# Kernel optimization log

Measured on AMD Instinct MI355X. Metric: run time of the kernel, lower is better.

## Reference

```python
import jax, jax.numpy as jnp
import numpy as np

N = 50000          # nodes
E = 800000         # edges per meta-path (avg degree 16)
M = 2              # meta-paths
IN = 256           # in_size
H, D = 4, 64       # heads, out_size per head
HD = H * D
SEM_HID = 128      # SemanticAttention hidden_size
NEG_SLOPE = 0.2    # DGL GATConv default LeakyReLU slope


def setup_inputs() -> dict:
    key = jax.random.key(0)
    ks = jax.random.split(key, 10)
    h = jax.random.normal(ks[0], (N, IN), dtype=jnp.float32)
    src = jax.random.randint(ks[1], (M, E), 0, N, dtype=jnp.int32)
    dst = jax.random.randint(ks[2], (M, E), 0, N, dtype=jnp.int32)
    # per-meta-path GATConv params
    W = jax.random.normal(ks[3], (M, IN, HD), dtype=jnp.float32) * (1.0 / np.sqrt(IN))
    attn_l = jax.random.normal(ks[4], (M, H, D), dtype=jnp.float32) * 0.1
    attn_r = jax.random.normal(ks[5], (M, H, D), dtype=jnp.float32) * 0.1
    # semantic attention params
    sem_w1 = jax.random.normal(ks[6], (HD, SEM_HID), dtype=jnp.float32) * (1.0 / np.sqrt(HD))
    sem_b1 = jnp.zeros((SEM_HID,), dtype=jnp.float32)
    sem_w2 = jax.random.normal(ks[7], (SEM_HID, 1), dtype=jnp.float32) * (1.0 / np.sqrt(SEM_HID))
    return {"h": h, "src": src, "dst": dst, "W": W, "attn_l": attn_l,
            "attn_r": attn_r, "sem_w1": sem_w1, "sem_b1": sem_b1, "sem_w2": sem_w2}


def _gat_conv(h, s, d, W_i, al, ar):
    # h: [N, IN]; s, d: [E] int edge endpoints; returns [N, H*D]
    feat = (h @ W_i).reshape(N, H, D)                       # [N,H,D]
    el = jnp.einsum('nhd,hd->nh', feat, al)                 # [N,H]
    er = jnp.einsum('nhd,hd->nh', feat, ar)                 # [N,H]
    e = jax.nn.leaky_relu(el[s] + er[d], NEG_SLOPE)         # [E,H]
    # edge softmax over incoming edges of each dst node
    m = jax.ops.segment_max(e, d, num_segments=N)           # [N,H]
    m = jax.lax.stop_gradient(jnp.where(jnp.isfinite(m), m, 0.0))
    ex = jnp.exp(e - m[d])                                  # [E,H]
    den = jax.ops.segment_sum(ex, d, num_segments=N)        # [N,H]
    alpha = ex / jnp.maximum(den[d], 1e-9)                  # [E,H]
    msg = alpha[:, :, None] * feat[s]                       # [E,H,D]
    rst = jax.ops.segment_sum(msg, d, num_segments=N)       # [N,H,D] (zero for 0-in-degree)
    return jax.nn.elu(rst).reshape(N, HD)


def reference(h, src, dst, W, attn_l, attn_r, sem_w1, sem_b1, sem_w2):
    embs = [_gat_conv(h, src[i], dst[i], W[i], attn_l[i], attn_r[i]) for i in range(M)]
    z = jnp.stack(embs, axis=1)                             # [N,M,HD]
    # semantic attention: w = mean over nodes of MLP score per meta-path
    w = jnp.einsum('nms,so->mo', jnp.tanh(jnp.einsum('nmd,ds->nms', z, sem_w1) + sem_b1), sem_w2) / N  # [M,1]
    beta = jax.nn.softmax(w, axis=0)                        # [M,1]
    return jnp.einsum('nmd,mo->nd', z, beta)                # [N,HD]
```

## Files before the change

### kernel.cpp

```cpp
#include <hip/hip_runtime.h>
#include <hip/hip_bf16.h>

#define NND 50000
#define NE 800000
#define NM 2
#define INF 256
#define NH 4
#define HDIM 256
#define SHID 128
#define SLOPE 0.2f
#define NB 196

typedef unsigned short u16;
typedef __attribute__((ext_vector_type(8))) short bf16x8;
typedef __attribute__((ext_vector_type(4))) float f32x4;

__device__ __forceinline__ float us2f(u16 u) {
  union { unsigned int i; float f; } v; v.i = ((unsigned int)u) << 16; return v.f;
}
__device__ __forceinline__ u16 f2us(float f) {
  union { float f; unsigned int i; } v; v.f = f;
  unsigned int r = v.i + 0x7FFFu + ((v.i >> 16) & 1u);
  return (u16)(r >> 16);
}

#define GLDS(g, l) __builtin_amdgcn_global_load_lds( \
    (const __attribute__((address_space(1))) unsigned int*)(g), \
    (__attribute__((address_space(3))) unsigned int*)(l), 16, 0, 0)

__global__ __launch_bounds__(256) void kh_cvt(const float* __restrict__ h,
                                              u16* __restrict__ hb) {
  const size_t i = ((size_t)blockIdx.x * 256 + threadIdx.x) * 8;
  float4 a = *(const float4*)(h + i);
  float4 b = *(const float4*)(h + i + 4);
  bf16x8 r;
  r[0] = f2us(a.x); r[1] = f2us(a.y); r[2] = f2us(a.z); r[3] = f2us(a.w);
  r[4] = f2us(b.x); r[5] = f2us(b.y); r[6] = f2us(b.z); r[7] = f2us(b.w);
  *(bf16x8*)(hb + i) = r;
}

__global__ __launch_bounds__(256) void kt_w(const float* __restrict__ W,
                                            u16* __restrict__ Wt) {
  __shared__ u16 tile[64][65];
  const int t = threadIdx.x;
  const int k0 = blockIdx.x * 64, n0 = blockIdx.y * 64;
  const float* Wm = W + (size_t)blockIdx.z * 65536;
  u16* Wtm = Wt + (size_t)blockIdx.z * 65536;
  const int lr = t >> 2, c0 = (t & 3) * 16;
#pragma unroll
  for (int i = 0; i < 16; ++i)
    tile[lr][c0 + i] = f2us(Wm[(size_t)(k0 + lr) * 256 + n0 + c0 + i]);
  __syncthreads();
#pragma unroll
  for (int i = 0; i < 16; ++i)
    Wtm[(size_t)(n0 + lr) * 256 + k0 + c0 + i] = tile[c0 + i][lr];
}

__global__ __launch_bounds__(256) void kt_w1(const float* __restrict__ w1,
                                             u16* __restrict__ w1t) {
  __shared__ u16 tile[64][65];
  const int t = threadIdx.x;
  const int k0 = blockIdx.x * 64, j0 = blockIdx.y * 64;
  const int lr = t >> 2, c0 = (t & 3) * 16;
#pragma unroll
  for (int i = 0; i < 16; ++i)
    tile[lr][c0 + i] = f2us(w1[(size_t)(k0 + lr) * SHID + j0 + c0 + i]);
  __syncthreads();
#pragma unroll
  for (int i = 0; i < 16; ++i)
    w1t[(size_t)(j0 + lr) * 256 + k0 + c0 + i] = tile[c0 + i][lr];
}

__global__ __launch_bounds__(256) void kc_hist(const int* __restrict__ dst,
                                               int* __restrict__ rowptr) {
  int e = blockIdx.x * 256 + threadIdx.x;
  if (e < NE) atomicAdd(rowptr + dst[e] + 1, 1);
}

__global__ __launch_bounds__(256) void ks1(int* __restrict__ rowptr,
                                           int* __restrict__ bsum) {
  __shared__ int wsums[4];
  const int t = threadIdx.x;
  const int i = blockIdx.x * 256 + t + 1;
  int v = (i <= NND) ? rowptr[i] : 0;
  const int lane = t & 63, wid = t >> 6;
#pragma unroll
  for (int o = 1; o < 64; o <<= 1) {
    int u = __shfl_up(v, o, 64);
    if (lane >= o) v += u;
  }
  if (lane == 63) wsums[wid] = v;
  __syncthreads();
  if (t == 0) {
    int s = 0;
#pragma unroll
    for (int w = 0; w < 4; ++w) { int x = wsums[w]; wsums[w] = s; s += x; }
    bsum[blockIdx.x] = s;
  }
  __syncthreads();
  v += wsums[wid];
  if (i <= NND) rowptr[i] = v;
}

__global__ __launch_bounds__(256) void ks2(int* __restrict__ bsum) {
  __shared__ int wsums[4];
  const int t = threadIdx.x;
  const int v0 = (t < NB) ? bsum[t] : 0;
  int v = v0;
  const int lane = t & 63, wid = t >> 6;
#pragma unroll
  for (int o = 1; o < 64; o <<= 1) {
    int u = __shfl_up(v, o, 64);
    if (lane >= o) v += u;
  }
  if (lane == 63) wsums[wid] = v;
  __syncthreads();
  if (t == 0) {
    int s = 0;
#pragma unroll
    for (int w = 0; w < 4; ++w) { int x = wsums[w]; wsums[w] = s; s += x; }
  }
  __syncthreads();
  v += wsums[wid];
  if (t < NB) bsum[t] = v - v0;
}

__global__ __launch_bounds__(256) void ks3(int* __restrict__ rowptr,
                                           const int* __restrict__ bsum) {
  const int i = blockIdx.x * 256 + threadIdx.x + 1;
  if (blockIdx.x > 0 && i <= NND) rowptr[i] += bsum[blockIdx.x];
}

__global__ __launch_bounds__(256) void kc_scatter(
    const int* __restrict__ src, const int* __restrict__ dst,
    int* __restrict__ cursor, int* __restrict__ col,
    const float* __restrict__ el, const float* __restrict__ er,
    float* __restrict__ exps)
{
  int e = blockIdx.x * 256 + threadIdx.x;
  if (e >= NE) return;
  int s = src[e], d = dst[e];
  int pos = atomicAdd(cursor + d, 1);
  col[pos] = s;
  float4 a = *(const float4*)(el + s * 4);
  float4 b = *(const float4*)(er + d * 4);
  float4 r;
  float x;
  x = a.x + b.x; x = x > 0.f ? x : SLOPE * x; r.x = __expf(x);
  x = a.y + b.y; x = x > 0.f ? x : SLOPE * x; r.y = __expf(x);
  x = a.z + b.z; x = x > 0.f ? x : SLOPE * x; r.z = __expf(x);
  x = a.w + b.w; x = x > 0.f ? x : SLOPE * x; r.w = __expf(x);
  *(float4*)(exps + (size_t)pos * 4) = r;
}

__global__ __launch_bounds__(256) void k1_mfma(
    const u16* __restrict__ hb, const u16* __restrict__ Wt,
    u16* __restrict__ feat)
{
  __shared__ u16 As[128 * 32];
  __shared__ u16 Bs[128 * 32];
  const int t = threadIdx.x;
  const int lane = t & 63;
  const int w = t >> 6;
  const int wr = w >> 1, wc = w & 1;
  const int row0 = blockIdx.x * 128;
  const int col0 = blockIdx.y * 128;

  const int sr = t >> 2;
  const int skb = (t & 3) * 8;

  int ra0 = row0 + sr;       if (ra0 >= NND) ra0 = NND - 1;
  int ra1 = row0 + 64 + sr;  if (ra1 >= NND) ra1 = NND - 1;
  const int cb0 = col0 + sr, cb1 = col0 + 64 + sr;

  f32x4 acc[4][4];
#pragma unroll
  for (int i = 0; i < 4; ++i)
#pragma unroll
    for (int j = 0; j < 4; ++j) acc[i][j] = (f32x4){0.f, 0.f, 0.f, 0.f};

  for (int ks = 0; ks < 8; ++ks) {
    const int kb = ks * 32 + skb;
    __syncthreads();
    GLDS(hb + (size_t)ra0 * INF + kb, As + w * 512);
    GLDS(hb + (size_t)ra1 * INF + kb, As + 2048 + w * 512);
    GLDS(Wt + (size_t)cb0 * 256 + kb, Bs + w * 512);
    GLDS(Wt + (size_t)cb1 * 256 + kb, Bs + 2048 + w * 512);
    __syncthreads();
    bf16x8 af[4], bfr[4];
#pragma unroll
    for (int mi = 0; mi < 4; ++mi)
      af[mi] = *(const bf16x8*)(As + (wr * 64 + mi * 16 + (lane & 15)) * 32 + (lane >> 4) * 8);
#pragma unroll
    for (int ni = 0; ni < 4; ++ni)
      bfr[ni] = *(const bf16x8*)(Bs + (wc * 64 + ni * 16 + (lane & 15)) * 32 + (lane >> 4) * 8);
#pragma unroll
    for (int mi = 0; mi < 4; ++mi)
#pragma unroll
      for (int ni = 0; ni < 4; ++ni)
        acc[mi][ni] = __builtin_amdgcn_mfma_f32_16x16x32_bf16(af[mi], bfr[ni], acc[mi][ni], 0, 0, 0);
  }
#pragma unroll
  for (int mi = 0; mi < 4; ++mi) {
    const int r_base = row0 + wr * 64 + mi * 16 + (lane >> 4) * 4;
#pragma unroll
    for (int i = 0; i < 4; ++i) {
      const int r = r_base + i;
      if (r < NND) {
#pragma unroll
        for (int ni = 0; ni < 4; ++ni) {
          const int c = col0 + wc * 64 + ni * 16 + (lane & 15);
          feat[(size_t)r * HDIM + c] = f2us(acc[mi][ni][i]);
        }
      }
    }
  }
}

__global__ __launch_bounds__(256) void k1b_elr(
    const u16* __restrict__ feat,
    const float* __restrict__ al, const float* __restrict__ ar,
    float* __restrict__ el, float* __restrict__ er)
{
  const int n = blockIdx.x * 4 + (threadIdx.x >> 6);
  const int lane = threadIdx.x & 63;
  ushort4 f4 = *(const ushort4*)(feat + (size_t)n * HDIM + lane * 4);
  float4 a4 = *(const float4*)(al + lane * 4);
  float4 r4 = *(const float4*)(ar + lane * 4);
  float fl = us2f(f4.x) * a4.x + us2f(f4.y) * a4.y
           + us2f(f4.z) * a4.z + us2f(f4.w) * a4.w;
  float fr = us2f(f4.x) * r4.x + us2f(f4.y) * r4.y
           + us2f(f4.z) * r4.z + us2f(f4.w) * r4.w;
#pragma unroll
  for (int o = 1; o < 16; o <<= 1) {
    fl += __shfl_xor(fl, o, 64);
    fr += __shfl_xor(fr, o, 64);
  }
  if ((lane & 15) == 0) {
    el[n * 4 + (lane >> 4)] = fl;
    er[n * 4 + (lane >> 4)] = fr;
  }
}

template<int OBF>
__global__ __launch_bounds__(256) void k3_gather(
    const int* __restrict__ rowptr, const int* __restrict__ col,
    const float* __restrict__ exps,
    const u16* __restrict__ feat, void* __restrict__ z)
{
  const int d = blockIdx.x * 4 + (threadIdx.x >> 6);
  if (d >= NND) return;
  const int lane = threadIdx.x & 63;
  const int h = lane >> 4;
  const int sub = lane & 15;
  const int beg = rowptr[d], end = rowptr[d + 1];

  float den = 0.f;
  for (int j = beg + sub; j < end; j += 16)
    den += exps[(size_t)j * 4 + h];
#pragma unroll
  for (int o = 1; o < 16; o <<= 1) den += __shfl_xor(den, o, 64);
  const float inv = 1.f / fmaxf(den, 1e-9f);

  float a0 = 0.f, a1 = 0.f, a2 = 0.f, a3 = 0.f;
  int j = beg;
  for (; j + 3 < end; j += 4) {
    int s0 = col[j], s1 = col[j + 1], s2 = col[j + 2], s3 = col[j + 3];
    float p0 = exps[(size_t)j * 4 + h] * inv;
    float p1 = exps[(size_t)(j + 1) * 4 + h] * inv;
    float p2 = exps[(size_t)(j + 2) * 4 + h] * inv;
    float p3 = exps[(size_t)(j + 3) * 4 + h] * inv;
    const ushort4 f0 = *(const ushort4*)(feat + (size_t)s0 * HDIM + lane * 4);
    const ushort4 f1 = *(const ushort4*)(feat + (size_t)s1 * HDIM + lane * 4);
    const ushort4 f2 = *(const ushort4*)(feat + (size_t)s2 * HDIM + lane * 4);
    const ushort4 f3 = *(const ushort4*)(feat + (size_t)s3 * HDIM + lane * 4);
    a0 = fmaf(p0, us2f(f0.x), a0); a1 = fmaf(p0, us2f(f0.y), a1);
    a2 = fmaf(p0, us2f(f0.z), a2); a3 = fmaf(p0, us2f(f0.w), a3);
    a0 = fmaf(p1, us2f(f1.x), a0); a1 = fmaf(p1, us2f(f1.y), a1);
    a2 = fmaf(p1, us2f(f1.z), a2); a3 = fmaf(p1, us2f(f1.w), a3);
    a0 = fmaf(p2, us2f(f2.x), a0); a1 = fmaf(p2, us2f(f2.y), a1);
    a2 = fmaf(p2, us2f(f2.z), a2); a3 = fmaf(p2, us2f(f2.w), a3);
    a0 = fmaf(p3, us2f(f3.x), a0); a1 = fmaf(p3, us2f(f3.y), a1);
    a2 = fmaf(p3, us2f(f3.z), a2); a3 = fmaf(p3, us2f(f3.w), a3);
  }
  for (; j < end; ++j) {
    int s = col[j];
    float p = exps[(size_t)j * 4 + h] * inv;
    const ushort4 f4 = *(const ushort4*)(feat + (size_t)s * HDIM + lane * 4);
    a0 = fmaf(p, us2f(f4.x), a0); a1 = fmaf(p, us2f(f4.y), a1);
    a2 = fmaf(p, us2f(f4.z), a2); a3 = fmaf(p, us2f(f4.w), a3);
  }
  a0 = a0 > 0.f ? a0 : expf(a0) - 1.f;
  a1 = a1 > 0.f ? a1 : expf(a1) - 1.f;
  a2 = a2 > 0.f ? a2 : expf(a2) - 1.f;
  a3 = a3 > 0.f ? a3 : expf(a3) - 1.f;
  const size_t idx = (size_t)d * HDIM + lane * 4;
  if (OBF) {
    ushort4 r; r.x = f2us(a0); r.y = f2us(a1); r.z = f2us(a2); r.w = f2us(a3);
    *(ushort4*)((u16*)z + idx) = r;
  } else {
    float4 r; r.x = a0; r.y = a1; r.z = a2; r.w = a3;
    *(float4*)((float*)z + idx) = r;
  }
}

template<int ZBF>
__global__ __launch_bounds__(256) void k4_mfma(
    const void* __restrict__ zsrc, const u16* __restrict__ w1t,
    const float* __restrict__ b1, const float* __restrict__ w2,
    float* __restrict__ wsum, int midx)
{
  __shared__ u16 As[128 * 32];
  __shared__ u16 Bs[128 * 32];
  __shared__ float red[4];
  const int t = threadIdx.x;
  const int lane = t & 63;
  const int w = t >> 6;
  const int wr = w >> 1, wc = w & 1;
  const int row0 = blockIdx.x * 128;
  const int sr = t >> 2;
  const int skb = (t & 3) * 8;
  int ra0 = row0 + sr;       if (ra0 >= NND) ra0 = NND - 1;
  int ra1 = row0 + 64 + sr;  if (ra1 >= NND) ra1 = NND - 1;
  const int cb0 = sr, cb1 = 64 + sr;

  f32x4 acc[4][4];
#pragma unroll
  for (int i = 0; i < 4; ++i)
#pragma unroll
    for (int j = 0; j < 4; ++j) acc[i][j] = (f32x4){0.f, 0.f, 0.f, 0.f};

  for (int ks = 0; ks < 8; ++ks) {
    const int kb = ks * 32 + skb;
    __syncthreads();
    if (ZBF) {
      GLDS((const u16*)zsrc + (size_t)ra0 * HDIM + kb, As + w * 512);
      GLDS((const u16*)zsrc + (size_t)ra1 * HDIM + kb, As + 2048 + w * 512);
    } else {
      const float* zf = (const float*)zsrc;
      float4 a = *(const float4*)(zf + (size_t)ra0 * HDIM + kb);
      float4 b = *(const float4*)(zf + (size_t)ra0 * HDIM + kb + 4);
      bf16x8 r;
      r[0] = f2us(a.x); r[1] = f2us(a.y); r[2] = f2us(a.z); r[3] = f2us(a.w);
      r[4] = f2us(b.x); r[5] = f2us(b.y); r[6] = f2us(b.z); r[7] = f2us(b.w);
      *(bf16x8*)(As + sr * 32 + skb) = r;
      a = *(const float4*)(zf + (size_t)ra1 * HDIM + kb);
      b = *(const float4*)(zf + (size_t)ra1 * HDIM + kb + 4);
      r[0] = f2us(a.x); r[1] = f2us(a.y); r[2] = f2us(a.z); r[3] = f2us(a.w);
      r[4] = f2us(b.x); r[5] = f2us(b.y); r[6] = f2us(b.z); r[7] = f2us(b.w);
      *(bf16x8*)(As + (64 + sr) * 32 + skb) = r;
    }
    GLDS(w1t + (size_t)cb0 * 256 + kb, Bs + w * 512);
    GLDS(w1t + (size_t)cb1 * 256 + kb, Bs + 2048 + w * 512);
    __syncthreads();
    bf16x8 af[4], bfr[4];
#pragma unroll
    for (int mi = 0; mi < 4; ++mi)
      af[mi] = *(const bf16x8*)(As + (wr * 64 + mi * 16 + (lane & 15)) * 32 + (lane >> 4) * 8);
#pragma unroll
    for (int ni = 0; ni < 4; ++ni)
      bfr[ni] = *(const bf16x8*)(Bs + (wc * 64 + ni * 16 + (lane & 15)) * 32 + (lane >> 4) * 8);
#pragma unroll
    for (int mi = 0; mi < 4; ++mi)
#pragma unroll
      for (int ni = 0; ni < 4; ++ni)
        acc[mi][ni] = __builtin_amdgcn_mfma_f32_16x16x32_bf16(af[mi], bfr[ni], acc[mi][ni], 0, 0, 0);
  }
  float sum = 0.f;
#pragma unroll
  for (int ni = 0; ni < 4; ++ni) {
    const int c = wc * 64 + ni * 16 + (lane & 15);
    const float b1c = b1[c], w2c = w2[c];
#pragma unroll
    for (int mi = 0; mi < 4; ++mi) {
      const int r_base = row0 + wr * 64 + mi * 16 + (lane >> 4) * 4;
#pragma unroll
      for (int i = 0; i < 4; ++i) {
        if (r_base + i < NND)
          sum += tanhf(acc[mi][ni][i] + b1c) * w2c;
      }
    }
  }
#pragma unroll
  for (int o = 32; o; o >>= 1) sum += __shfl_xor(sum, o, 64);
  if (lane == 0) red[w] = sum;
  __syncthreads();
  if (t == 0) unsafeAtomicAdd(wsum + midx, red[0] + red[1] + red[2] + red[3]);
}

__global__ __launch_bounds__(256) void k5_out(
    float* __restrict__ out, const u16* __restrict__ z1,
    const float* __restrict__ wsum)
{
  const int i = blockIdx.x * 256 + threadIdx.x;
  float w0 = wsum[0] * (1.0f / NND);
  float w1v = wsum[1] * (1.0f / NND);
  float mx = fmaxf(w0, w1v);
  float e0 = expf(w0 - mx), e1 = expf(w1v - mx);
  float inv = 1.f / (e0 + e1);
  float b0 = e0 * inv, b1 = e1 * inv;
  float4 a = ((const float4*)out)[i];
  ushort4 zb = ((const ushort4*)z1)[i];
  float4 r;
  r.x = b0 * a.x + b1 * us2f(zb.x);
  r.y = b0 * a.y + b1 * us2f(zb.y);
  r.z = b0 * a.z + b1 * us2f(zb.z);
  r.w = b0 * a.w + b1 * us2f(zb.w);
  ((float4*)out)[i] = r;
}

extern "C" void kernel_launch(void* const* d_in, const int* in_sizes, int n_in,
                              void* d_out, int out_size, void* d_ws, size_t ws_size,
                              hipStream_t stream)
{
  const float* h  = (const float*)d_in[0];
  const int* src  = (const int*)d_in[1];
  const int* dst  = (const int*)d_in[2];
  const float* W  = (const float*)d_in[3];
  const float* al = (const float*)d_in[4];
  const float* ar = (const float*)d_in[5];
  const float* w1 = (const float*)d_in[6];
  const float* b1 = (const float*)d_in[7];
  const float* w2 = (const float*)d_in[8];

  char* wsb = (char*)d_ws;
  u16*   feat   = (u16*)(wsb);
  u16*   hz     = (u16*)(wsb + 25600000);
  float* exps   = (float*)(wsb + 51200000);
  int*   col    = (int*)(wsb + 64000000);
  u16*   Wt     = (u16*)(wsb + 67200000);
  u16*   w1t    = (u16*)(wsb + 67462144);
  float* el     = (float*)(wsb + 67527680);
  float* er     = (float*)(wsb + 68327680);
  int*   rowptr = (int*)(wsb + 69127680);
  int*   cursor = (int*)(wsb + 69327684);
  float* wsum   = (float*)(wsb + 69527684);
  int*   bsum   = (int*)(wsb + 69527696);
  const size_t NEED = 69528480;
  if (ws_size < NEED) {
    hipMemsetAsync(d_out, 0x7F, (size_t)out_size * 4, stream);
    return;
  }
  u16* z1 = hz;
  float* outp = (float*)d_out;

  kh_cvt<<<6250, 256, 0, stream>>>(h, hz);
  kt_w<<<dim3(4, 4, 2), 256, 0, stream>>>(W, Wt);
  kt_w1<<<dim3(4, 2), 256, 0, stream>>>(w1, w1t);
  hipMemsetAsync(wsum, 0, 2 * sizeof(float), stream);
  for (int m = 0; m < NM; ++m) {
    const int* src_m = src + (size_t)m * NE;
    const int* dst_m = dst + (size_t)m * NE;
    k1_mfma<<<dim3(391, 2), 256, 0, stream>>>(hz, Wt + (size_t)m * 65536, feat);
    k1b_elr<<<12500, 256, 0, stream>>>(feat, al + (size_t)m * HDIM, ar + (size_t)m * HDIM, el, er);
    hipMemsetAsync(rowptr, 0, (NND + 1) * sizeof(int), stream);
    kc_hist<<<NE / 256, 256, 0, stream>>>(dst_m, rowptr);
    ks1<<<NB, 256, 0, stream>>>(rowptr, bsum);
    ks2<<<1, 256, 0, stream>>>(bsum);
    ks3<<<NB, 256, 0, stream>>>(rowptr, bsum);
    hipMemcpyAsync(cursor, rowptr, NND * sizeof(int), hipMemcpyDeviceToDevice, stream);
    kc_scatter<<<NE / 256, 256, 0, stream>>>(src_m, dst_m, cursor, col, el, er, exps);
    if (m == 0) {
      k3_gather<0><<<12500, 256, 0, stream>>>(rowptr, col, exps, feat, d_out);
      k4_mfma<0><<<391, 256, 0, stream>>>(d_out, w1t, b1, w2, wsum, 0);
    } else {
      k3_gather<1><<<12500, 256, 0, stream>>>(rowptr, col, exps, feat, z1);
      k4_mfma<1><<<391, 256, 0, stream>>>(z1, w1t, b1, w2, wsum, 1);
    }
  }
  k5_out<<<(NND * HDIM / 4) / 256, 256, 0, stream>>>(outp, z1, wsum);
}
```

Baseline: 443.8 us.

## Fuse el/er into GEMM epilogue, widen gather loads, fold cursor copy into scan

The feature GEMM now computes all 256 output columns per block and reduces the attention dot products el/er in its epilogue, which removes the separate k1b_elr pass over feat. The gather kernel splits each wave into two halves that process alternate edges with 16-byte bf16x8 loads, then combines the halves with a cross-half shuffle. The cursor copy is folded into ks3, and the two per-metapath rowptr buffers are zeroed with a single memset. In exchange, the wider GEMM tile raises register and LDS pressure and halves the grid size.

```diff
diff --git a/kernel.cpp b/kernel.cpp
--- a/kernel.cpp
+++ b/kernel.cpp
@@ -126,9 +126,14 @@
 }
 
 __global__ __launch_bounds__(256) void ks3(int* __restrict__ rowptr,
-                                           const int* __restrict__ bsum) {
+                                           const int* __restrict__ bsum,
+                                           int* __restrict__ cursor) {
   const int i = blockIdx.x * 256 + threadIdx.x + 1;
-  if (blockIdx.x > 0 && i <= NND) rowptr[i] += bsum[blockIdx.x];
+  if (i > NND) return;
+  int v = rowptr[i];
+  if (blockIdx.x > 0) { v += bsum[blockIdx.x]; rowptr[i] = v; }
+  if (i < NND) cursor[i] = v;
+  if (i == 1) cursor[0] = 0;
 }
 
 __global__ __launch_bounds__(256) void kc_scatter(
@@ -155,90 +160,91 @@
 
 __global__ __launch_bounds__(256) void k1_mfma(
     const u16* __restrict__ hb, const u16* __restrict__ Wt,
-    u16* __restrict__ feat)
+    const float* __restrict__ al, const float* __restrict__ ar,
+    u16* __restrict__ feat, float* __restrict__ el, float* __restrict__ er)
 {
   __shared__ u16 As[128 * 32];
-  __shared__ u16 Bs[128 * 32];
+  __shared__ u16 Bs[256 * 32];
   const int t = threadIdx.x;
   const int lane = t & 63;
   const int w = t >> 6;
   const int wr = w >> 1, wc = w & 1;
   const int row0 = blockIdx.x * 128;
-  const int col0 = blockIdx.y * 128;
 
   const int sr = t >> 2;
   const int skb = (t & 3) * 8;
 
   int ra0 = row0 + sr;       if (ra0 >= NND) ra0 = NND - 1;
   int ra1 = row0 + 64 + sr;  if (ra1 >= NND) ra1 = NND - 1;
-  const int cb0 = col0 + sr, cb1 = col0 + 64 + sr;
-
-  f32x4 acc[4][4];
+
+  f32x4 acc[4][8];
 #pragma unroll
   for (int i = 0; i < 4; ++i)
 #pragma unroll
-    for (int j = 0; j < 4; ++j) acc[i][j] = (f32x4){0.f, 0.f, 0.f, 0.f};
+    for (int j = 0; j < 8; ++j) acc[i][j] = (f32x4){0.f, 0.f, 0.f, 0.f};
 
   for (int ks = 0; ks < 8; ++ks) {
     const int kb = ks * 32 + skb;
     __syncthreads();
     GLDS(hb + (size_t)ra0 * INF + kb, As + w * 512);
     GLDS(hb + (size_t)ra1 * INF + kb, As + 2048 + w * 512);
-    GLDS(Wt + (size_t)cb0 * 256 + kb, Bs + w * 512);
-    GLDS(Wt + (size_t)cb1 * 256 + kb, Bs + 2048 + w * 512);
+    GLDS(Wt + (size_t)sr * 256 + kb,         Bs + w * 512);
+    GLDS(Wt + (size_t)(64 + sr) * 256 + kb,  Bs + 2048 + w * 512);
+    GLDS(Wt + (size_t)(128 + sr) * 256 + kb, Bs + 4096 + w * 512);
+    GLDS(Wt + (size_t)(192 + sr) * 256 + kb, Bs + 6144 + w * 512);
     __syncthreads();
-    bf16x8 af[4], bfr[4];
+    bf16x8 af[4], bfr[8];
 #pragma unroll
     for (int mi = 0; mi < 4; ++mi)
       af[mi] = *(const bf16x8*)(As + (wr * 64 + mi * 16 + (lane & 15)) * 32 + (lane >> 4) * 8);
 #pragma unroll
-    for (int ni = 0; ni < 4; ++ni)
-      bfr[ni] = *(const bf16x8*)(Bs + (wc * 64 + ni * 16 + (lane & 15)) * 32 + (lane >> 4) * 8);
+    for (int ni = 0; ni < 8; ++ni)
+      bfr[ni] = *(const bf16x8*)(Bs + (wc * 128 + ni * 16 + (lane & 15)) * 32 + (lane >> 4) * 8);
 #pragma unroll
     for (int mi = 0; mi < 4; ++mi)
 #pragma unroll
-      for (int ni = 0; ni < 4; ++ni)
+      for (int ni = 0; ni < 8; ++ni)
         acc[mi][ni] = __builtin_amdgcn_mfma_f32_16x16x32_bf16(af[mi], bfr[ni], acc[mi][ni], 0, 0, 0);
   }
+  float alc[8], arc[8];
+#pragma unroll
+  for (int ni = 0; ni < 8; ++ni) {
+    const int c = wc * 128 + ni * 16 + (lane & 15);
+    alc[ni] = al[c]; arc[ni] = ar[c];
+  }
 #pragma unroll
   for (int mi = 0; mi < 4; ++mi) {
-    const int r_base = row0 + wr * 64 + mi * 16 + (lane >> 4) * 4;
 #pragma unroll
     for (int i = 0; i < 4; ++i) {
-      const int r = r_base + i;
-      if (r < NND) {
-#pragma unroll
-        for (int ni = 0; ni < 4; ++ni) {
-          const int c = col0 + wc * 64 + ni * 16 + (lane & 15);
-          feat[(size_t)r * HDIM + c] = f2us(acc[mi][ni][i]);
-        }
+      const int r = row0 + wr * 64 + mi * 16 + (lane >> 4) * 4 + i;
+      const bool valid = (r < NND);
+      float pel0 = 0.f, per0 = 0.f, pel1 = 0.f, per1 = 0.f;
+#pragma unroll
+      for (int ni = 0; ni < 4; ++ni) {
+        float fe = acc[mi][ni][i];
+        if (valid)
+          feat[(size_t)r * HDIM + wc * 128 + ni * 16 + (lane & 15)] = f2us(fe);
+        pel0 = fmaf(fe, alc[ni], pel0); per0 = fmaf(fe, arc[ni], per0);
+      }
+#pragma unroll
+      for (int ni = 4; ni < 8; ++ni) {
+        float fe = acc[mi][ni][i];
+        if (valid)
+          feat[(size_t)r * HDIM + wc * 128 + ni * 16 + (lane & 15)] = f2us(fe);
+        pel1 = fmaf(fe, alc[ni], pel1); per1 = fmaf(fe, arc[ni], per1);
+      }
+#pragma unroll
+      for (int o = 1; o < 16; o <<= 1) {
+        pel0 += __shfl_xor(pel0, o, 64);
+        per0 += __shfl_xor(per0, o, 64);
+        pel1 += __shfl_xor(pel1, o, 64);
+        per1 += __shfl_xor(per1, o, 64);
+      }
+      if (valid && (lane & 15) == 0) {
+        el[r * 4 + 2 * wc]     = pel0;  er[r * 4 + 2 * wc]     = per0;
+        el[r * 4 + 2 * wc + 1] = pel1;  er[r * 4 + 2 * wc + 1] = per1;
       }
     }
-  }
-}
-
-__global__ __launch_bounds__(256) void k1b_elr(
-    const u16* __restrict__ feat,
-    const float* __restrict__ al, const float* __restrict__ ar,
-    float* __restrict__ el, float* __restrict__ er)
-{
-  const int n = blockIdx.x * 4 + (threadIdx.x >> 6);
-  const int lane = threadIdx.x & 63;
-  ushort4 f4 = *(const ushort4*)(feat + (size_t)n * HDIM + lane * 4);
-  float4 a4 = *(const float4*)(al + lane * 4);
-  float4 r4 = *(const float4*)(ar + lane * 4);
-  float fl = us2f(f4.x) * a4.x + us2f(f4.y) * a4.y
-           + us2f(f4.z) * a4.z + us2f(f4.w) * a4.w;
-  float fr = us2f(f4.x) * r4.x + us2f(f4.y) * r4.y
-           + us2f(f4.z) * r4.z + us2f(f4.w) * r4.w;
-#pragma unroll
-  for (int o = 1; o < 16; o <<= 1) {
-    fl += __shfl_xor(fl, o, 64);
-    fr += __shfl_xor(fr, o, 64);
-  }
-  if ((lane & 15) == 0) {
-    el[n * 4 + (lane >> 4)] = fl;
-    er[n * 4 + (lane >> 4)] = fr;
   }
 }
 
@@ -251,56 +257,69 @@
   const int d = blockIdx.x * 4 + (threadIdx.x >> 6);
   if (d >= NND) return;
   const int lane = threadIdx.x & 63;
-  const int h = lane >> 4;
-  const int sub = lane & 15;
+  const int half = lane >> 5;
+  const int s32 = lane & 31;
+  const int h8 = s32 >> 3;
   const int beg = rowptr[d], end = rowptr[d + 1];
 
   float den = 0.f;
-  for (int j = beg + sub; j < end; j += 16)
-    den += exps[(size_t)j * 4 + h];
-#pragma unroll
-  for (int o = 1; o < 16; o <<= 1) den += __shfl_xor(den, o, 64);
-  const float inv = 1.f / fmaxf(den, 1e-9f);
+  {
+    const int hd = lane >> 4, sub = lane & 15;
+    for (int j = beg + sub; j < end; j += 16)
+      den += exps[(size_t)j * 4 + hd];
+#pragma unroll
+    for (int o = 1; o < 16; o <<= 1) den += __shfl_xor(den, o, 64);
+  }
+  const float inv = 1.f / fmaxf(__shfl(den, h8 * 16, 64), 1e-9f);
 
   float a0 = 0.f, a1 = 0.f, a2 = 0.f, a3 = 0.f;
-  int j = beg;
-  for (; j + 3 < end; j += 4) {
-    int s0 = col[j], s1 = col[j + 1], s2 = col[j + 2], s3 = col[j + 3];
-    float p0 = exps[(size_t)j * 4 + h] * inv;
-    float p1 = exps[(size_t)(j + 1) * 4 + h] * inv;
-    float p2 = exps[(size_t)(j + 2) * 4 + h] * inv;
-    float p3 = exps[(size_t)(j + 3) * 4 + h] * inv;
-    const ushort4 f0 = *(const ushort4*)(feat + (size_t)s0 * HDIM + lane * 4);
-    const ushort4 f1 = *(const ushort4*)(feat + (size_t)s1 * HDIM + lane * 4);
-    const ushort4 f2 = *(const ushort4*)(feat + (size_t)s2 * HDIM + lane * 4);
-    const ushort4 f3 = *(const ushort4*)(feat + (size_t)s3 * HDIM + lane * 4);
-    a0 = fmaf(p0, us2f(f0.x), a0); a1 = fmaf(p0, us2f(f0.y), a1);
-    a2 = fmaf(p0, us2f(f0.z), a2); a3 = fmaf(p0, us2f(f0.w), a3);
-    a0 = fmaf(p1, us2f(f1.x), a0); a1 = fmaf(p1, us2f(f1.y), a1);
-    a2 = fmaf(p1, us2f(f1.z), a2); a3 = fmaf(p1, us2f(f1.w), a3);
-    a0 = fmaf(p2, us2f(f2.x), a0); a1 = fmaf(p2, us2f(f2.y), a1);
-    a2 = fmaf(p2, us2f(f2.z), a2); a3 = fmaf(p2, us2f(f2.w), a3);
-    a0 = fmaf(p3, us2f(f3.x), a0); a1 = fmaf(p3, us2f(f3.y), a1);
-    a2 = fmaf(p3, us2f(f3.z), a2); a3 = fmaf(p3, us2f(f3.w), a3);
-  }
-  for (; j < end; ++j) {
-    int s = col[j];
-    float p = exps[(size_t)j * 4 + h] * inv;
-    const ushort4 f4 = *(const ushort4*)(feat + (size_t)s * HDIM + lane * 4);
-    a0 = fmaf(p, us2f(f4.x), a0); a1 = fmaf(p, us2f(f4.y), a1);
-    a2 = fmaf(p, us2f(f4.z), a2); a3 = fmaf(p, us2f(f4.w), a3);
-  }
-  a0 = a0 > 0.f ? a0 : expf(a0) - 1.f;
-  a1 = a1 > 0.f ? a1 : expf(a1) - 1.f;
-  a2 = a2 > 0.f ? a2 : expf(a2) - 1.f;
-  a3 = a3 > 0.f ? a3 : expf(a3) - 1.f;
-  const size_t idx = (size_t)d * HDIM + lane * 4;
-  if (OBF) {
-    ushort4 r; r.x = f2us(a0); r.y = f2us(a1); r.z = f2us(a2); r.w = f2us(a3);
-    *(ushort4*)((u16*)z + idx) = r;
-  } else {
-    float4 r; r.x = a0; r.y = a1; r.z = a2; r.w = a3;
-    *(float4*)((float*)z + idx) = r;
+  float a4 = 0.f, a5 = 0.f, a6 = 0.f, a7 = 0.f;
+  int j = beg + half;
+  for (; j + 2 < end; j += 4) {
+    const int s0 = col[j], s1 = col[j + 2];
+    const float p0 = exps[(size_t)j * 4 + h8] * inv;
+    const float p1 = exps[(size_t)(j + 2) * 4 + h8] * inv;
+    const bf16x8 f0 = *(const bf16x8*)(feat + (size_t)s0 * HDIM + s32 * 8);
+    const bf16x8 f1 = *(const bf16x8*)(feat + (size_t)s1 * HDIM + s32 * 8);
+    a0 = fmaf(p0, us2f((u16)f0[0]), a0); a1 = fmaf(p0, us2f((u16)f0[1]), a1);
+    a2 = fmaf(p0, us2f((u16)f0[2]), a2); a3 = fmaf(p0, us2f((u16)f0[3]), a3);
+    a4 = fmaf(p0, us2f((u16)f0[4]), a4); a5 = fmaf(p0, us2f((u16)f0[5]), a5);
+    a6 = fmaf(p0, us2f((u16)f0[6]), a6); a7 = fmaf(p0, us2f((u16)f0[7]), a7);
+    a0 = fmaf(p1, us2f((u16)f1[0]), a0); a1 = fmaf(p1, us2f((u16)f1[1]), a1);
+    a2 = fmaf(p1, us2f((u16)f1[2]), a2); a3 = fmaf(p1, us2f((u16)f1[3]), a3);
+    a4 = fmaf(p1, us2f((u16)f1[4]), a4); a5 = fmaf(p1, us2f((u16)f1[5]), a5);
+    a6 = fmaf(p1, us2f((u16)f1[6]), a6); a7 = fmaf(p1, us2f((u16)f1[7]), a7);
+  }
+  for (; j < end; j += 2) {
+    const int s = col[j];
+    const float p = exps[(size_t)j * 4 + h8] * inv;
+    const bf16x8 f = *(const bf16x8*)(feat + (size_t)s * HDIM + s32 * 8);
+    a0 = fmaf(p, us2f((u16)f[0]), a0); a1 = fmaf(p, us2f((u16)f[1]), a1);
+    a2 = fmaf(p, us2f((u16)f[2]), a2); a3 = fmaf(p, us2f((u16)f[3]), a3);
+    a4 = fmaf(p, us2f((u16)f[4]), a4); a5 = fmaf(p, us2f((u16)f[5]), a5);
+    a6 = fmaf(p, us2f((u16)f[6]), a6); a7 = fmaf(p, us2f((u16)f[7]), a7);
+  }
+  a0 += __shfl_xor(a0, 32, 64); a1 += __shfl_xor(a1, 32, 64);
+  a2 += __shfl_xor(a2, 32, 64); a3 += __shfl_xor(a3, 32, 64);
+  a4 += __shfl_xor(a4, 32, 64); a5 += __shfl_xor(a5, 32, 64);
+  a6 += __shfl_xor(a6, 32, 64); a7 += __shfl_xor(a7, 32, 64);
+  if (half == 0) {
+    a0 = a0 > 0.f ? a0 : expf(a0) - 1.f;  a1 = a1 > 0.f ? a1 : expf(a1) - 1.f;
+    a2 = a2 > 0.f ? a2 : expf(a2) - 1.f;  a3 = a3 > 0.f ? a3 : expf(a3) - 1.f;
+    a4 = a4 > 0.f ? a4 : expf(a4) - 1.f;  a5 = a5 > 0.f ? a5 : expf(a5) - 1.f;
+    a6 = a6 > 0.f ? a6 : expf(a6) - 1.f;  a7 = a7 > 0.f ? a7 : expf(a7) - 1.f;
+    const size_t idx = (size_t)d * HDIM + s32 * 8;
+    if (OBF) {
+      bf16x8 r;
+      r[0] = f2us(a0); r[1] = f2us(a1); r[2] = f2us(a2); r[3] = f2us(a3);
+      r[4] = f2us(a4); r[5] = f2us(a5); r[6] = f2us(a6); r[7] = f2us(a7);
+      *(bf16x8*)((u16*)z + idx) = r;
+    } else {
+      float4 r0; r0.x = a0; r0.y = a1; r0.z = a2; r0.w = a3;
+      float4 r1; r1.x = a4; r1.y = a5; r1.z = a6; r1.w = a7;
+      *(float4*)((float*)z + idx) = r0;
+      *(float4*)((float*)z + idx + 4) = r1;
+    }
   }
 }
 
@@ -433,10 +452,10 @@
   float* el     = (float*)(wsb + 67527680);
   float* er     = (float*)(wsb + 68327680);
   int*   rowptr = (int*)(wsb + 69127680);
-  int*   cursor = (int*)(wsb + 69327684);
-  float* wsum   = (float*)(wsb + 69527684);
-  int*   bsum   = (int*)(wsb + 69527696);
-  const size_t NEED = 69528480;
+  int*   cursor = (int*)(wsb + 69527688);
+  float* wsum   = (float*)(wsb + 69727688);
+  int*   bsum   = (int*)(wsb + 69727696);
+  const size_t NEED = 69728480;
   if (ws_size < NEED) {
     hipMemsetAsync(d_out, 0x7F, (size_t)out_size * 4, stream);
     return;
@@ -448,23 +467,24 @@
   kt_w<<<dim3(4, 4, 2), 256, 0, stream>>>(W, Wt);
   kt_w1<<<dim3(4, 2), 256, 0, stream>>>(w1, w1t);
   hipMemsetAsync(wsum, 0, 2 * sizeof(float), stream);
+  hipMemsetAsync(rowptr, 0, 2 * (NND + 1) * sizeof(int), stream);
   for (int m = 0; m < NM; ++m) {
     const int* src_m = src + (size_t)m * NE;
     const int* dst_m = dst + (size_t)m * NE;
-    k1_mfma<<<dim3(391, 2), 256, 0, stream>>>(hz, Wt + (size_t)m * 65536, feat);
-    k1b_elr<<<12500, 256, 0, stream>>>(feat, al + (size_t)m * HDIM, ar + (size_t)m * HDIM, el, er);
-    hipMemsetAsync(rowptr, 0, (NND + 1) * sizeof(int), stream);
-    kc_hist<<<NE / 256, 256, 0, stream>>>(dst_m, rowptr);
-    ks1<<<NB, 256, 0, stream>>>(rowptr, bsum);
+    int* rowptr_m = rowptr + (size_t)m * (NND + 1);
+    k1_mfma<<<391, 256, 0, stream>>>(hz, Wt + (size_t)m * 65536,
+                                     al + (size_t)m * HDIM, ar + (size_t)m * HDIM,
+                                     feat, el, er);
+    kc_hist<<<NE / 256, 256, 0, stream>>>(dst_m, rowptr_m);
+    ks1<<<NB, 256, 0, stream>>>(rowptr_m, bsum);
     ks2<<<1, 256, 0, stream>>>(bsum);
-    ks3<<<NB, 256, 0, stream>>>(rowptr, bsum);
-    hipMemcpyAsync(cursor, rowptr, NND * sizeof(int), hipMemcpyDeviceToDevice, stream);
+    ks3<<<NB, 256, 0, stream>>>(rowptr_m, bsum, cursor);
     kc_scatter<<<NE / 256, 256, 0, stream>>>(src_m, dst_m, cursor, col, el, er, exps);
     if (m == 0) {
-      k3_gather<0><<<12500, 256, 0, stream>>>(rowptr, col, exps, feat, d_out);
+      k3_gather<0><<<12500, 256, 0, stream>>>(rowptr_m, col, exps, feat, d_out);
       k4_mfma<0><<<391, 256, 0, stream>>>(d_out, w1t, b1, w2, wsum, 0);
     } else {
-      k3_gather<1><<<12500, 256, 0, stream>>>(rowptr, col, exps, feat, z1);
+      k3_gather<1><<<12500, 256, 0, stream>>>(rowptr_m, col, exps, feat, z1);
       k4_mfma<1><<<391, 256, 0, stream>>>(z1, w1t, b1, w2, wsum, 1);
     }
   }
```

Result: slower. 453.8 us (+2.3%).
